# Kernel tuning notes

Measured on AMD Instinct MI355X. Metric: run time of the kernel, lower is better.

## Reference

```python
import jax, jax.numpy as jnp
import numpy as np
from itertools import product

D = 128      # full-resolution voxel grid extent
DP = 64      # pooled grid extent (stride 2)
M = 131072   # number of pooled (output) voxels
CH = 2       # children per pooled cell
N = M * CH   # number of input active voxels = 262144
EPS = 1e-5


def _build_maps():
    rng = np.random.default_rng(0)
    plin = rng.choice(DP ** 3, size=M, replace=False).astype(np.int64)
    px = plin // (DP * DP); py = (plin // DP) % DP; pz = plin % DP
    pcoords = np.stack([px, py, pz], 1)                      # [M,3]
    off8 = np.array(list(product([0, 1], repeat=3)), np.int64)   # [8,3]
    sel = np.argsort(rng.random((M, 8)), 1)[:, :CH]          # pick 2 of 8 children
    coords = (pcoords[:, None, :] * 2 + off8[sel]).reshape(-1, 3)  # [N,3]

    def make_lookup(c, d):
        lin = (c[:, 0] * d + c[:, 1]) * d + c[:, 2]
        order = np.argsort(lin); slin = lin[order]
        def lookup(q):
            inb = np.all((q >= 0) & (q < d), 1)
            ql = (q[:, 0] * d + q[:, 1]) * d + q[:, 2]
            pos = np.searchsorted(slin, ql)
            pos_c = np.clip(pos, 0, len(slin) - 1)
            found = inb & (slin[pos_c] == ql)
            return np.where(found, order[pos_c], -1).astype(np.int32)
        return lookup

    lk_full = make_lookup(coords, D)
    lk_pool = make_lookup(pcoords, DP)
    off27 = np.array(list(product([-1, 0, 1], repeat=3)), np.int64)  # [27,3]
    nbr1 = np.stack([lk_full(coords + o) for o in off27])            # [27,N]
    pool_map = np.stack([lk_full(pcoords * 2 + o) for o in off8])    # [8,M]
    nbr2 = np.stack([lk_pool(pcoords + o) for o in off27])           # [27,M]
    return nbr1, pool_map, nbr2


def setup_inputs() -> dict:
    nbr1, pool_map, nbr2 = _build_maps()
    key = jax.random.key(0)
    k1, k2, k3, k4 = jax.random.split(key, 4)
    feats = jax.random.normal(k1, (N, 3), jnp.float32)
    # kaiming-ish scaling over fan_in = 27*Cin
    W1 = jax.random.normal(k2, (27, 3, 64), jnp.float32) * np.sqrt(2.0 / (27 * 3))
    W2 = jax.random.normal(k3, (27, 64, 64), jnp.float32) * np.sqrt(2.0 / (27 * 64))
    W3 = jax.random.normal(k4, (27, 64, 128), jnp.float32) * np.sqrt(2.0 / (27 * 64))
    return {"feats": feats, "W1": W1, "W2": W2, "W3": W3,
            "nbr1": jnp.asarray(nbr1), "pool_map": jnp.asarray(pool_map),
            "nbr2": jnp.asarray(nbr2)}


def sparse_conv(x, W, nbr):
    """Gather-GEMM-scatter sparse conv. x:[Nin,Cin], W:[K,Cin,Cout], nbr:[K,Nout]."""
    out = jnp.zeros((nbr.shape[1], W.shape[-1]), x.dtype)
    for k in range(W.shape[0]):           # fixed small loop over 27 kernel offsets
        idx = nbr[k]
        m = (idx >= 0)
        g = x[jnp.where(m, idx, 0)] * m[:, None].astype(x.dtype)  # [Nout,Cin]
        out = out + g @ W[k]
    return out


def inst_norm(x):
    mu = jnp.mean(x, axis=0, keepdims=True)
    var = jnp.var(x, axis=0, keepdims=True)
    return (x - mu) / jnp.sqrt(var + EPS)


def max_pool(x, pool_map):
    out = jnp.full((pool_map.shape[1], x.shape[1]), -jnp.inf, x.dtype)
    for o in range(pool_map.shape[0]):    # 8 pooling offsets
        idx = pool_map[o]
        m = (idx >= 0)
        g = jnp.where(m[:, None], x[jnp.where(m, idx, 0)], -jnp.inf)
        out = jnp.maximum(out, g)
    return out


def reference(feats, W1, W2, W3, nbr1, pool_map, nbr2):
    x = jax.nn.relu(inst_norm(sparse_conv(feats, W1, nbr1)))  # [N,64]
    x = jax.nn.relu(inst_norm(sparse_conv(x, W2, nbr1)))      # [N,64]
    x = max_pool(x, pool_map)                                  # [M,64]
    x = jax.nn.relu(inst_norm(sparse_conv(x, W3, nbr2)))      # [M,128]
    return x
```

## Files before the change

### kernel.cpp

```cpp
#include <hip/hip_runtime.h>
#include <hip/hip_bf16.h>

#define N_FULL 262144
#define M_POOL 131072

typedef __attribute__((ext_vector_type(4))) float f32x4;
typedef __attribute__((ext_vector_type(8))) short bf16x8;
typedef __attribute__((ext_vector_type(8))) unsigned short u16x8;

static __device__ __forceinline__ unsigned short f2b(float f) {
    __hip_bfloat16 b = __float2bfloat16(f);
    return *reinterpret_cast<unsigned short*>(&b);
}
static __device__ __forceinline__ float b2f(unsigned short u) {
    unsigned int x = ((unsigned int)u) << 16;
    return __uint_as_float(x);
}

static __device__ __forceinline__ void gll16(const void* g, void* l) {
    __builtin_amdgcn_global_load_lds(
        (const __attribute__((address_space(1))) void*)g,
        (__attribute__((address_space(3))) void*)l, 16, 0, 0);
}

template<int CT, int NPT>
__global__ __launch_bounds__(256) void pack_w_kernel(const float* __restrict__ W,
                                                     unsigned short* __restrict__ Wp) {
    int i = blockIdx.x * 256 + threadIdx.x;
    const int total = NPT * 2 * CT * 64 * 8;
    if (i >= total) return;
    int j = i & 7;
    int l = (i >> 3) & 63;
    int t = (i >> 9) % CT;
    int q = (i / (512 * CT)) & 1;
    int k = i / (1024 * CT);
    int cin = q * 32 + (l >> 4) * 8 + j;
    int cout = t * 16 + (l & 15);
    float v = (k < 27) ? W[(k * 64 + cin) * (CT * 16) + cout] : 0.f;
    Wp[i] = f2b(v);
}

__global__ __launch_bounds__(256) void pack_w1_kernel(const float* __restrict__ W1,
                                                      unsigned short* __restrict__ Wp) {
    int i = blockIdx.x * 256 + threadIdx.x;
    const int total = 7 * 4 * 64 * 8;
    if (i >= total) return;
    int j = i & 7;
    int l = (i >> 3) & 63;
    int t = (i >> 9) & 3;
    int kb = i >> 11;
    int tap = kb * 4 + (l >> 4);
    float v = 0.f;
    if (tap < 27 && j < 3) v = W1[(tap * 3 + j) * 64 + t * 16 + (l & 15)];
    Wp[i] = f2b(v);
}

__global__ __launch_bounds__(256) void pack_feats_kernel(const float* __restrict__ feats,
                                                         unsigned short* __restrict__ fp, int N) {
    int i = blockIdx.x * 256 + threadIdx.x;
    if (i > N) return;
    ushort4 o;
    if (i < N) {
        o.x = f2b(feats[(size_t)i * 3 + 0]);
        o.y = f2b(feats[(size_t)i * 3 + 1]);
        o.z = f2b(feats[(size_t)i * 3 + 2]);
        o.w = 0;
    } else { o.x = o.y = o.z = o.w = 0; }
    reinterpret_cast<ushort4*>(fp)[i] = o;
}

__global__ __launch_bounds__(256) void conv1_mfma_kernel(const unsigned short* __restrict__ fp,
                                                         const unsigned short* __restrict__ Wp,
                                                         const int* __restrict__ nbr,
                                                         unsigned short* __restrict__ Y,
                                                         float* __restrict__ sums, int R) {
    __shared__ unsigned short lw[7 * 2048];
    __shared__ float psum[4][64], psq[4][64];
    const int tid = threadIdx.x;
    const int wave = tid >> 6;
    const int lane = tid & 63;
    const int l16 = lane & 15;
    const int lq = lane >> 4;
    const int rowbase = blockIdx.x * 128 + wave * 32;
    const int zrow = R;

    {
        const char* gsrc = (const char*)Wp;
        char* lbase = (char*)lw;
        #pragma unroll
        for (int c = 0; c < 7; ++c) {
            int off = (wave * 7 + c) * 1024;
            gll16(gsrc + off + lane * 16, lbase + off);
        }
    }
    int idx[7][2];
    #pragma unroll
    for (int g = 0; g < 7; ++g) {
        int tap = g * 4 + lq; if (tap > 26) tap = 26;
        #pragma unroll
        for (int s = 0; s < 2; ++s) {
            int v = nbr[(size_t)tap * R + rowbase + s * 16 + l16];
            idx[g][s] = ((g * 4 + lq) > 26 || v < 0) ? zrow : v;
        }
    }
    bf16x8 af[7][2];
    #pragma unroll
    for (int g = 0; g < 7; ++g)
        #pragma unroll
        for (int s = 0; s < 2; ++s) {
            short4 v = *reinterpret_cast<const short4*>(fp + (size_t)idx[g][s] * 4);
            af[g][s][0] = v.x; af[g][s][1] = v.y; af[g][s][2] = v.z; af[g][s][3] = v.w;
            af[g][s][4] = 0; af[g][s][5] = 0; af[g][s][6] = 0; af[g][s][7] = 0;
        }
    __syncthreads();

    f32x4 acc[2][4];
    #pragma unroll
    for (int s = 0; s < 2; ++s)
        #pragma unroll
        for (int t = 0; t < 4; ++t)
            #pragma unroll
            for (int g = 0; g < 4; ++g) acc[s][t][g] = 0.f;

    #pragma unroll
    for (int g = 0; g < 7; ++g) {
        #pragma unroll
        for (int t = 0; t < 4; ++t) {
            bf16x8 bfr = *reinterpret_cast<const bf16x8*>(&lw[g * 2048 + t * 512 + lane * 8]);
            #pragma unroll
            for (int s = 0; s < 2; ++s)
                acc[s][t] = __builtin_amdgcn_mfma_f32_16x16x32_bf16(af[g][s], bfr, acc[s][t], 0, 0, 0);
        }
    }
    #pragma unroll
    for (int t = 0; t < 4; ++t) {
        float s1 = 0.f, s2 = 0.f;
        #pragma unroll
        for (int s = 0; s < 2; ++s)
            #pragma unroll
            for (int g = 0; g < 4; ++g) {
                float v = acc[s][t][g];
                s1 += v; s2 += v * v;
                Y[(size_t)(rowbase + s * 16 + lq * 4 + g) * 64 + t * 16 + l16] = f2b(v);
            }
        s1 += __shfl_xor(s1, 16); s2 += __shfl_xor(s2, 16);
        s1 += __shfl_xor(s1, 32); s2 += __shfl_xor(s2, 32);
        if (lq == 0) { psum[wave][t * 16 + l16] = s1; psq[wave][t * 16 + l16] = s2; }
    }
    __syncthreads();
    if (tid < 64) {
        float s1 = 0.f, s2 = 0.f;
        #pragma unroll
        for (int w = 0; w < 4; ++w) { s1 += psum[w][tid]; s2 += psq[w][tid]; }
        atomicAdd(&sums[tid], s1);
        atomicAdd(&sums[64 + tid], s2);
    }
}

template<int CT, int TCH, int NPT>
__global__ __launch_bounds__(256) void conv_mfma_kernel(const unsigned short* __restrict__ X,
                                                        const unsigned short* __restrict__ Wp,
                                                        const int* __restrict__ nbr,
                                                        unsigned short* __restrict__ Y,
                                                        float* __restrict__ sums, int Nout) {
    constexpr int C = CT * 16;
    constexpr int NPH = NPT / TCH;
    constexpr int TAPW = CT * 1024;
    constexpr int PHW = TCH * TAPW;
    constexpr int SCH = TCH * CT / 2;
    __shared__ unsigned short lw[PHW];
    __shared__ float psum[4][C], psq[4][C];
    const int tid = threadIdx.x;
    const int wave = tid >> 6;
    const int lane = tid & 63;
    const int l16 = lane & 15;
    const int lq = lane >> 4;
    const int rowbase = blockIdx.x * 128 + wave * 32;

    f32x4 acc[2][CT];
    #pragma unroll
    for (int s = 0; s < 2; ++s)
        #pragma unroll
        for (int t = 0; t < CT; ++t)
            #pragma unroll
            for (int g = 0; g < 4; ++g) acc[s][t][g] = 0.f;
    bf16x8 zf;
    #pragma unroll
    for (int j = 0; j < 8; ++j) zf[j] = 0;

    int idxp[TCH][2];
    #pragma unroll
    for (int t = 0; t < TCH; ++t)
        #pragma unroll
        for (int s = 0; s < 2; ++s)
            idxp[t][s] = nbr[(size_t)t * Nout + rowbase + s * 16 + l16];

    for (int ph = 0; ph < NPH; ++ph) {
        if (ph) __syncthreads();
        {
            const char* gseg = (const char*)(Wp + (size_t)ph * PHW);
            char* lbase = (char*)lw;
            const int woff = wave * (SCH * 1024);
            #pragma unroll
            for (int c = 0; c < SCH; ++c) {
                int off = woff + c * 1024;
                gll16(gseg + off + lane * 16, lbase + off);
            }
        }
        bf16x8 af[TCH][2][2];
        #pragma unroll
        for (int t = 0; t < TCH; ++t)
            #pragma unroll
            for (int s = 0; s < 2; ++s) {
                int ic = idxp[t][s];
                #pragma unroll
                for (int q = 0; q < 2; ++q) af[t][s][q] = zf;
                if (ic >= 0) {
                    #pragma unroll
                    for (int q = 0; q < 2; ++q)
                        af[t][s][q] = *reinterpret_cast<const bf16x8*>(
                            X + (size_t)ic * 64 + q * 32 + lq * 8);
                }
            }
        int idxn[TCH][2];
        #pragma unroll
        for (int t = 0; t < TCH; ++t) {
            int tap = (ph + 1) * TCH + t; if (tap > 26) tap = 26;
            #pragma unroll
            for (int s = 0; s < 2; ++s)
                idxn[t][s] = nbr[(size_t)tap * Nout + rowbase + s * 16 + l16];
        }
        __syncthreads();
        #pragma unroll
        for (int t = 0; t < TCH; ++t)
            #pragma unroll
            for (int q = 0; q < 2; ++q)
                #pragma unroll
                for (int tt = 0; tt < CT; ++tt) {
                    bf16x8 bfr = *reinterpret_cast<const bf16x8*>(
                        &lw[t * TAPW + (q * CT + tt) * 512 + lane * 8]);
                    #pragma unroll
                    for (int s = 0; s < 2; ++s)
                        acc[s][tt] = __builtin_amdgcn_mfma_f32_16x16x32_bf16(
                            af[t][s][q], bfr, acc[s][tt], 0, 0, 0);
                }
        #pragma unroll
        for (int t = 0; t < TCH; ++t)
            #pragma unroll
            for (int s = 0; s < 2; ++s) idxp[t][s] = idxn[t][s];
    }
    #pragma unroll
    for (int t = 0; t < CT; ++t) {
        float s1 = 0.f, s2 = 0.f;
        #pragma unroll
        for (int s = 0; s < 2; ++s)
            #pragma unroll
            for (int g = 0; g < 4; ++g) {
                float v = acc[s][t][g];
                s1 += v; s2 += v * v;
                Y[(size_t)(rowbase + s * 16 + lq * 4 + g) * C + t * 16 + l16] = f2b(v);
            }
        s1 += __shfl_xor(s1, 16); s2 += __shfl_xor(s2, 16);
        s1 += __shfl_xor(s1, 32); s2 += __shfl_xor(s2, 32);
        if (lq == 0) { psum[wave][t * 16 + l16] = s1; psq[wave][t * 16 + l16] = s2; }
    }
    __syncthreads();
    if (tid < C) {
        float s1 = 0.f, s2 = 0.f;
        #pragma unroll
        for (int w = 0; w < 4; ++w) { s1 += psum[w][tid]; s2 += psq[w][tid]; }
        atomicAdd(&sums[tid], s1);
        atomicAdd(&sums[C + tid], s2);
    }
}

template<int C>
__global__ __launch_bounds__(256) void norm_bf16_kernel(const unsigned short* __restrict__ Y,
                                                        const float* __restrict__ sums,
                                                        unsigned short* __restrict__ Xb, int R) {
    __shared__ float lmu[C], lrs[C];
    if (threadIdx.x < C) {
        float m = sums[threadIdx.x] / (float)R;
        float v = sums[C + threadIdx.x] / (float)R - m * m;
        lmu[threadIdx.x] = m;
        lrs[threadIdx.x] = rsqrtf(fmaxf(v, 0.f) + 1e-5f);
    }
    __syncthreads();
    const int total = R * C / 8;
    for (int i = blockIdx.x * 256 + threadIdx.x; i < total; i += gridDim.x * 256) {
        u16x8 v = reinterpret_cast<const u16x8*>(Y)[i];
        int cb = (i * 8) & (C - 1);
        u16x8 o;
        #pragma unroll
        for (int j = 0; j < 8; ++j) {
            float f = b2f(v[j]);
            o[j] = f2b(fmaxf((f - lmu[cb + j]) * lrs[cb + j], 0.f));
        }
        reinterpret_cast<u16x8*>(Xb)[i] = o;
    }
}

template<int C>
__global__ __launch_bounds__(256) void norm_f32_kernel(const unsigned short* __restrict__ Y,
                                                       const float* __restrict__ sums,
                                                       float* __restrict__ Out, int R) {
    __shared__ float lmu[C], lrs[C];
    if (threadIdx.x < C) {
        float m = sums[threadIdx.x] / (float)R;
        float v = sums[C + threadIdx.x] / (float)R - m * m;
        lmu[threadIdx.x] = m;
        lrs[threadIdx.x] = rsqrtf(fmaxf(v, 0.f) + 1e-5f);
    }
    __syncthreads();
    const int total = R * C / 8;
    for (int i = blockIdx.x * 256 + threadIdx.x; i < total; i += gridDim.x * 256) {
        u16x8 v = reinterpret_cast<const u16x8*>(Y)[i];
        int cb = (i * 8) & (C - 1);
        float4 o0, o1;
        o0.x = fmaxf((b2f(v[0]) - lmu[cb + 0]) * lrs[cb + 0], 0.f);
        o0.y = fmaxf((b2f(v[1]) - lmu[cb + 1]) * lrs[cb + 1], 0.f);
        o0.z = fmaxf((b2f(v[2]) - lmu[cb + 2]) * lrs[cb + 2], 0.f);
        o0.w = fmaxf((b2f(v[3]) - lmu[cb + 3]) * lrs[cb + 3], 0.f);
        o1.x = fmaxf((b2f(v[4]) - lmu[cb + 4]) * lrs[cb + 4], 0.f);
        o1.y = fmaxf((b2f(v[5]) - lmu[cb + 5]) * lrs[cb + 5], 0.f);
        o1.z = fmaxf((b2f(v[6]) - lmu[cb + 6]) * lrs[cb + 6], 0.f);
        o1.w = fmaxf((b2f(v[7]) - lmu[cb + 7]) * lrs[cb + 7], 0.f);
        reinterpret_cast<float4*>(Out)[i * 2] = o0;
        reinterpret_cast<float4*>(Out)[i * 2 + 1] = o1;
    }
}

__global__ __launch_bounds__(256) void pool_norm_kernel(const unsigned short* __restrict__ Y2,
                                                        const int* __restrict__ pmap,
                                                        const float* __restrict__ sums,
                                                        unsigned short* __restrict__ Xp,
                                                        int M, int R) {
    __shared__ float lmu[64], lrs[64];
    if (threadIdx.x < 64) {
        float m = sums[threadIdx.x] / (float)R;
        float v = sums[64 + threadIdx.x] / (float)R - m * m;
        lmu[threadIdx.x] = m;
        lrs[threadIdx.x] = rsqrtf(fmaxf(v, 0.f) + 1e-5f);
    }
    __syncthreads();
    const int lane = threadIdx.x & 63;
    const int gw = blockIdx.x * 4 + (threadIdx.x >> 6);
    const int nw = gridDim.x * 4;
    for (int m = gw; m < M; m += nw) {
        int idx[8];
        #pragma unroll
        for (int o = 0; o < 8; ++o) idx[o] = pmap[o * M + m];
        float best = -INFINITY;
        #pragma unroll
        for (int o = 0; o < 8; ++o)
            if (idx[o] >= 0) best = fmaxf(best, b2f(Y2[(size_t)idx[o] * 64 + lane]));
        Xp[(size_t)m * 64 + lane] = f2b(fmaxf((best - lmu[lane]) * lrs[lane], 0.f));
    }
}

extern "C" void kernel_launch(void* const* d_in, const int* in_sizes, int n_in,
                              void* d_out, int out_size, void* d_ws, size_t ws_size,
                              hipStream_t stream) {
    const float* feats = (const float*)d_in[0];
    const float* W1 = (const float*)d_in[1];
    const float* W2 = (const float*)d_in[2];
    const float* W3 = (const float*)d_in[3];
    const int* nbr1 = (const int*)d_in[4];
    const int* pmap = (const int*)d_in[5];
    const int* nbr2 = (const int*)d_in[6];
    float* out = (float*)d_out;

    const int N = N_FULL, M = M_POOL;
    char* ws = (char*)d_ws;
    unsigned short* yb = (unsigned short*)ws;
    unsigned short* xb = yb + (size_t)N * 64;
    unsigned short* fpk = xb + (size_t)N * 64;
    unsigned short* w1p = fpk + (size_t)(N + 1) * 4;
    unsigned short* w2p = w1p + 7 * 2048;
    unsigned short* w3p = w2p + 27 * 4096;
    float* sums = (float*)(w3p + 28 * 8192);
    float* sums1 = sums;
    float* sums2 = sums + 128;
    float* sums3 = sums + 256;

    hipMemsetAsync(sums, 0, 512 * sizeof(float), stream);
    pack_feats_kernel<<<(N + 256) / 256, 256, 0, stream>>>(feats, fpk, N);
    pack_w1_kernel<<<(7 * 2048 + 255) / 256, 256, 0, stream>>>(W1, w1p);
    pack_w_kernel<4, 27><<<(27 * 4096 + 255) / 256, 256, 0, stream>>>(W2, w2p);
    pack_w_kernel<8, 28><<<(28 * 8192 + 255) / 256, 256, 0, stream>>>(W3, w3p);

    conv1_mfma_kernel<<<N / 128, 256, 0, stream>>>(fpk, w1p, nbr1, yb, sums1, N);
    norm_bf16_kernel<64><<<2048, 256, 0, stream>>>(yb, sums1, xb, N);

    conv_mfma_kernel<4, 3, 27><<<N / 128, 256, 0, stream>>>(xb, w2p, nbr1, yb, sums2, N);
    pool_norm_kernel<<<2048, 256, 0, stream>>>(yb, pmap, sums2, xb, M, N);

    conv_mfma_kernel<8, 2, 28><<<M / 128, 256, 0, stream>>>(xb, w3p, nbr2, yb, sums3, M);
    norm_f32_kernel<128><<<2048, 256, 0, stream>>>(yb, sums3, out, M);
}
```

Before: 419.3 us.

## Software-pipeline neighbor gathers across taps with zero-row and larger weight groups

```diff
diff --git a/kernel.cpp b/kernel.cpp
--- a/kernel.cpp
+++ b/kernel.cpp
@@ -69,6 +69,10 @@
     reinterpret_cast<ushort4*>(fp)[i] = o;
 }
 
+__global__ void zero_row_kernel(unsigned short* __restrict__ xb) {
+    if (threadIdx.x < 64) xb[(size_t)N_FULL * 64 + threadIdx.x] = 0;
+}
+
 __global__ __launch_bounds__(256) void conv1_mfma_kernel(const unsigned short* __restrict__ fp,
                                                          const unsigned short* __restrict__ Wp,
                                                          const int* __restrict__ nbr,
@@ -157,18 +161,19 @@
     }
 }
 
-template<int CT, int TCH, int NPT>
+template<int CT, int GS, int NG>
 __global__ __launch_bounds__(256) void conv_mfma_kernel(const unsigned short* __restrict__ X,
                                                         const unsigned short* __restrict__ Wp,
                                                         const int* __restrict__ nbr,
                                                         unsigned short* __restrict__ Y,
-                                                        float* __restrict__ sums, int Nout) {
+                                                        float* __restrict__ sums,
+                                                        int Nout, int zrow) {
     constexpr int C = CT * 16;
-    constexpr int NPH = NPT / TCH;
+    constexpr int NT = GS * NG;
     constexpr int TAPW = CT * 1024;
-    constexpr int PHW = TCH * TAPW;
-    constexpr int SCH = TCH * CT / 2;
-    __shared__ unsigned short lw[PHW];
+    constexpr int GRPW = GS * TAPW;
+    constexpr int SCH = GS * CT / 2;
+    __shared__ unsigned short lw[GRPW];
     __shared__ float psum[4][C], psq[4][C];
     const int tid = threadIdx.x;
     const int wave = tid >> 6;
@@ -184,70 +189,83 @@
         for (int t = 0; t < CT; ++t)
             #pragma unroll
             for (int g = 0; g < 4; ++g) acc[s][t][g] = 0.f;
-    bf16x8 zf;
-    #pragma unroll
-    for (int j = 0; j < 8; ++j) zf[j] = 0;
-
-    int idxp[TCH][2];
-    #pragma unroll
-    for (int t = 0; t < TCH; ++t)
+
+    bf16x8 sa[3][2][2];
+    int si[4][2];
+
+    #pragma unroll
+    for (int k = 0; k < 4; ++k) {
+        int tp = k <= 26 ? k : 26;
         #pragma unroll
         for (int s = 0; s < 2; ++s)
-            idxp[t][s] = nbr[(size_t)t * Nout + rowbase + s * 16 + l16];
-
-    for (int ph = 0; ph < NPH; ++ph) {
-        if (ph) __syncthreads();
-        {
-            const char* gseg = (const char*)(Wp + (size_t)ph * PHW);
+            si[k][s] = nbr[(size_t)tp * Nout + rowbase + s * 16 + l16];
+    }
+    {
+        const char* gseg = (const char*)Wp;
+        char* lbase = (char*)lw;
+        #pragma unroll
+        for (int c = 0; c < SCH; ++c) {
+            int off = wave * (SCH * 1024) + c * 1024;
+            gll16(gseg + off + lane * 16, lbase + off);
+        }
+    }
+    #pragma unroll
+    for (int k = 0; k < 2; ++k)
+        #pragma unroll
+        for (int s = 0; s < 2; ++s) {
+            int ic = si[k][s] < 0 ? zrow : si[k][s];
+            const unsigned short* base = X + (size_t)ic * 64 + lq * 8;
+            sa[k][s][0] = *reinterpret_cast<const bf16x8*>(base);
+            sa[k][s][1] = *reinterpret_cast<const bf16x8*>(base + 32);
+        }
+    __syncthreads();
+
+    #pragma unroll
+    for (int g = 0; g < NG; ++g) {
+        if (g) {
+            __syncthreads();
+            const char* gseg = (const char*)(Wp + (size_t)g * GRPW);
             char* lbase = (char*)lw;
-            const int woff = wave * (SCH * 1024);
             #pragma unroll
             for (int c = 0; c < SCH; ++c) {
-                int off = woff + c * 1024;
+                int off = wave * (SCH * 1024) + c * 1024;
                 gll16(gseg + off + lane * 16, lbase + off);
             }
-        }
-        bf16x8 af[TCH][2][2];
-        #pragma unroll
-        for (int t = 0; t < TCH; ++t)
-            #pragma unroll
-            for (int s = 0; s < 2; ++s) {
-                int ic = idxp[t][s];
+            asm volatile("s_waitcnt vmcnt(0)" ::: "memory");
+            __builtin_amdgcn_s_barrier();
+            asm volatile("" ::: "memory");
+        }
+        #pragma unroll
+        for (int t = 0; t < GS; ++t) {
+            const int tap = g * GS + t;
+            if (tap + 2 < NT) {
                 #pragma unroll
-                for (int q = 0; q < 2; ++q) af[t][s][q] = zf;
-                if (ic >= 0) {
-                    #pragma unroll
-                    for (int q = 0; q < 2; ++q)
-                        af[t][s][q] = *reinterpret_cast<const bf16x8*>(
-                            X + (size_t)ic * 64 + q * 32 + lq * 8);
+                for (int s = 0; s < 2; ++s) {
+                    int iv = si[(tap + 2) & 3][s];
+                    int ic = iv < 0 ? zrow : iv;
+                    const unsigned short* base = X + (size_t)ic * 64 + lq * 8;
+                    sa[(tap + 2) % 3][s][0] = *reinterpret_cast<const bf16x8*>(base);
+                    sa[(tap + 2) % 3][s][1] = *reinterpret_cast<const bf16x8*>(base + 32);
                 }
             }
-        int idxn[TCH][2];
-        #pragma unroll
-        for (int t = 0; t < TCH; ++t) {
-            int tap = (ph + 1) * TCH + t; if (tap > 26) tap = 26;
-            #pragma unroll
-            for (int s = 0; s < 2; ++s)
-                idxn[t][s] = nbr[(size_t)tap * Nout + rowbase + s * 16 + l16];
-        }
-        __syncthreads();
-        #pragma unroll
-        for (int t = 0; t < TCH; ++t)
+            if (tap + 4 < NT) {
+                int tp = (tap + 4) <= 26 ? (tap + 4) : 26;
+                #pragma unroll
+                for (int s = 0; s < 2; ++s)
+                    si[(tap + 4) & 3][s] = nbr[(size_t)tp * Nout + rowbase + s * 16 + l16];
+            }
             #pragma unroll
             for (int q = 0; q < 2; ++q)
                 #pragma unroll
                 for (int tt = 0; tt < CT; ++tt) {
-                    bf16x8 bfr = *reinterpret_cast<const bf16x8*>(
+                    bf16x8 b = *reinterpret_cast<const bf16x8*>(
                         &lw[t * TAPW + (q * CT + tt) * 512 + lane * 8]);
                     #pragma unroll
                     for (int s = 0; s < 2; ++s)
                         acc[s][tt] = __builtin_amdgcn_mfma_f32_16x16x32_bf16(
-                            af[t][s][q], bfr, acc[s][tt], 0, 0, 0);
+                            sa[tap % 3][s][q], b, acc[s][tt], 0, 0, 0);
                 }
-        #pragma unroll
-        for (int t = 0; t < TCH; ++t)
-            #pragma unroll
-            for (int s = 0; s < 2; ++s) idxp[t][s] = idxn[t][s];
+        }
     }
     #pragma unroll
     for (int t = 0; t < CT; ++t) {
@@ -374,7 +392,7 @@
     char* ws = (char*)d_ws;
     unsigned short* yb = (unsigned short*)ws;
     unsigned short* xb = yb + (size_t)N * 64;
-    unsigned short* fpk = xb + (size_t)N * 64;
+    unsigned short* fpk = xb + (size_t)(N + 1) * 64;
     unsigned short* w1p = fpk + (size_t)(N + 1) * 4;
     unsigned short* w2p = w1p + 7 * 2048;
     unsigned short* w3p = w2p + 27 * 4096;
@@ -384,6 +402,7 @@
     float* sums3 = sums + 256;
 
     hipMemsetAsync(sums, 0, 512 * sizeof(float), stream);
+    zero_row_kernel<<<1, 64, 0, stream>>>(xb);
     pack_feats_kernel<<<(N + 256) / 256, 256, 0, stream>>>(feats, fpk, N);
     pack_w1_kernel<<<(7 * 2048 + 255) / 256, 256, 0, stream>>>(W1, w1p);
     pack_w_kernel<4, 27><<<(27 * 4096 + 255) / 256, 256, 0, stream>>>(W2, w2p);
@@ -392,9 +411,9 @@
     conv1_mfma_kernel<<<N / 128, 256, 0, stream>>>(fpk, w1p, nbr1, yb, sums1, N);
     norm_bf16_kernel<64><<<2048, 256, 0, stream>>>(yb, sums1, xb, N);
 
-    conv_mfma_kernel<4, 3, 27><<<N / 128, 256, 0, stream>>>(xb, w2p, nbr1, yb, sums2, N);
+    conv_mfma_kernel<4, 9, 3><<<N / 128, 256, 0, stream>>>(xb, w2p, nbr1, yb, sums2, N, N);
     pool_norm_kernel<<<2048, 256, 0, stream>>>(yb, pmap, sums2, xb, M, N);
 
-    conv_mfma_kernel<8, 2, 28><<<M / 128, 256, 0, stream>>>(xb, w3p, nbr2, yb, sums3, M);
+    conv_mfma_kernel<8, 4, 7><<<M / 128, 256, 0, stream>>>(xb, w3p, nbr2, yb, sums3, M, N);
     norm_f32_kernel<128><<<2048, 256, 0, stream>>>(yb, sums3, out, M);
 }
```

Result: slower. 443.3 us (+5.7%).
